# Optimization experiments

Hardware: AMD Instinct MI355X
Metric: run time of the kernel (lower is better)

The kernel has to match this reference:

```python
import jax, jax.numpy as jnp
import numpy as np

N_NODES = 50000
N_EDGES = 800000
IN_DIM = 128
HIDDEN = 64
HEADS = 4
EPS = 1e-5
NEG_SLOPE = 0.2  # PyG GATConv default


def setup_inputs() -> dict:
    key = jax.random.key(0)
    ks = jax.random.split(key, 12)
    s = 0.1
    x = jax.random.normal(ks[0], (N_NODES, IN_DIM), jnp.float32)
    edge_index = jax.random.randint(ks[1], (2, N_EDGES), 0, N_NODES, dtype=jnp.int64)
    return {
        "x": x,
        "edge_index": edge_index,
        # BatchNorm1d(input_dim)
        "gamma1": jnp.ones((IN_DIM,), jnp.float32),
        "beta1": jnp.zeros((IN_DIM,), jnp.float32),
        # GATConv(IN_DIM, HIDDEN, heads=HEADS, concat=True)
        "W1": jax.random.normal(ks[2], (IN_DIM, HEADS * HIDDEN), jnp.float32) * s,
        "att_src1": jax.random.normal(ks[3], (HEADS, HIDDEN), jnp.float32) * s,
        "att_dst1": jax.random.normal(ks[4], (HEADS, HIDDEN), jnp.float32) * s,
        "bias1": jnp.zeros((HEADS * HIDDEN,), jnp.float32),
        # BatchNorm1d(hidden*heads)
        "gamma2": jnp.ones((HEADS * HIDDEN,), jnp.float32),
        "beta2": jnp.zeros((HEADS * HIDDEN,), jnp.float32),
        # GATConv(hidden*heads, HIDDEN, heads=HEADS, concat=False)
        "W2": jax.random.normal(ks[5], (HEADS * HIDDEN, HEADS * HIDDEN), jnp.float32) * s,
        "att_src2": jax.random.normal(ks[6], (HEADS, HIDDEN), jnp.float32) * s,
        "att_dst2": jax.random.normal(ks[7], (HEADS, HIDDEN), jnp.float32) * s,
        "bias2": jnp.zeros((HIDDEN,), jnp.float32),
    }


def batchnorm(x, gamma, beta):
    # training-mode BatchNorm1d: biased variance over the batch dim
    m = x.mean(axis=0)
    v = x.var(axis=0)
    return (x - m) * jax.lax.rsqrt(v + EPS) * gamma + beta


def gat_conv(h, src, dst, W, att_src, att_dst, bias, concat):
    n = h.shape[0]
    hl = (h @ W).reshape(n, HEADS, -1)                 # [N, H, C]
    a_src = (hl * att_src).sum(-1)                     # [N, H]
    a_dst = (hl * att_dst).sum(-1)                     # [N, H]
    e = jax.nn.leaky_relu(a_src[src] + a_dst[dst], NEG_SLOPE)  # [E, H]
    # segment softmax over destination neighborhoods
    e_max = jax.ops.segment_max(e, dst, num_segments=n)
    e = jnp.exp(e - e_max[dst])
    denom = jax.ops.segment_sum(e, dst, num_segments=n)
    alpha = e / denom[dst]                             # [E, H]
    msg = alpha[:, :, None] * hl[src]                  # [E, H, C]
    out = jax.ops.segment_sum(msg, dst, num_segments=n)  # [N, H, C]
    out = out.reshape(n, -1) if concat else out.mean(axis=1)
    return out + bias


def reference(x, edge_index, gamma1, beta1, W1, att_src1, att_dst1, bias1,
              gamma2, beta2, W2, att_src2, att_dst2, bias2):
    n = x.shape[0]
    loop = jnp.arange(n, dtype=edge_index.dtype)
    src = jnp.concatenate([edge_index[0], loop])  # add_self_loops=True
    dst = jnp.concatenate([edge_index[1], loop])
    h = batchnorm(x, gamma1, beta1)
    h = gat_conv(h, src, dst, W1, att_src1, att_dst1, bias1, concat=True)
    h = batchnorm(h, gamma2, beta2)
    h = jax.nn.relu(h)
    h = gat_conv(h, src, dst, W2, att_src2, att_dst2, bias2, concat=False)
    return h
```

## Files before the change

### kernel.cpp

```cpp
#include <hip/hip_runtime.h>

#define N_NODES 50000
#define N_EDGES 800000
#define E_TOT   (N_EDGES + N_NODES)
#define F1      128
#define F2      256
#define EPS     1e-5f
#define SLOPE   0.2f
#define CAP     448
#define SCAN_B  256
#define N_BLKS  ((N_NODES + SCAN_B - 1) / SCAN_B)

typedef __bf16 bf16x8 __attribute__((ext_vector_type(8)));
typedef float  f32x4  __attribute__((ext_vector_type(4)));

__device__ __forceinline__ float bf2f(unsigned short b) {
    return __uint_as_float((unsigned)b << 16);
}

template<int C>
__global__ void bn_stats(const float* __restrict__ X,
                         float* __restrict__ sums, float* __restrict__ sumsq) {
    int t = threadIdx.x;
    float s = 0.f, q = 0.f;
    for (int r = blockIdx.x; r < N_NODES; r += gridDim.x) {
        float v = X[(size_t)r * C + t];
        s += v; q += v * v;
    }
    atomicAdd(&sums[t], s);
    atomicAdd(&sumsq[t], q);
}

__global__ void bn_coef(const float* __restrict__ sums, const float* __restrict__ sumsq,
                        const float* __restrict__ gamma, const float* __restrict__ beta,
                        float* __restrict__ scale, float* __restrict__ shift, int K) {
    int t = blockIdx.x * 64 + threadIdx.x;
    if (t < K) {
        const float invN = 1.f / (float)N_NODES;
        float m  = sums[t] * invN;
        float vv = sumsq[t] * invN - m * m;
        float sc = rsqrtf(vv + EPS) * gamma[t];
        scale[t] = sc;
        shift[t] = fmaf(-m, sc, beta[t]);
    }
}

__global__ void deg_init(int* __restrict__ deg) {
    int i = blockIdx.x * 256 + threadIdx.x;
    if (i < N_NODES) deg[i] = 1;
}
__global__ void deg_count(const int* __restrict__ edst, int* __restrict__ deg) {
    int i = blockIdx.x * 256 + threadIdx.x;
    if (i < N_EDGES) atomicAdd(&deg[edst[i]], 1);
}
__global__ void scan_blocks(const int* __restrict__ deg, int* __restrict__ rowptr,
                            int* __restrict__ bsum) {
    __shared__ int sd[SCAN_B];
    int b = blockIdx.x, t = threadIdx.x;
    int i = b * SCAN_B + t;
    int v = (i < N_NODES) ? deg[i] : 0;
    sd[t] = v;
    __syncthreads();
    for (int off = 1; off < SCAN_B; off <<= 1) {
        int x = (t >= off) ? sd[t - off] : 0;
        __syncthreads();
        sd[t] += x;
        __syncthreads();
    }
    if (i < N_NODES) rowptr[i + 1] = sd[t];
    if (t == SCAN_B - 1) bsum[b] = sd[t];
}
__global__ void scan_totals(int* __restrict__ bsum) {
    __shared__ int sd[SCAN_B];
    int t = threadIdx.x;
    int v = (t < N_BLKS) ? bsum[t] : 0;
    sd[t] = v;
    __syncthreads();
    for (int off = 1; off < SCAN_B; off <<= 1) {
        int x = (t >= off) ? sd[t - off] : 0;
        __syncthreads();
        sd[t] += x;
        __syncthreads();
    }
    if (t < N_BLKS) bsum[t] = sd[t] - v;
}
__global__ void scan_apply(const int* __restrict__ deg, const int* __restrict__ bsum,
                           int* __restrict__ rowptr, int* __restrict__ cursor) {
    int i = blockIdx.x * SCAN_B + threadIdx.x;
    if (i < N_NODES) {
        int r = rowptr[i + 1] + bsum[blockIdx.x];
        rowptr[i + 1] = r;
        cursor[i] = r - deg[i];
        if (i == 0) rowptr[0] = 0;
    }
}
__global__ void fill_csr(const int* __restrict__ esrc, const int* __restrict__ edst,
                         int* __restrict__ cursor, int* __restrict__ col) {
    int i = blockIdx.x * 256 + threadIdx.x;
    if (i < N_EDGES) {
        int p = atomicAdd(&cursor[edst[i]], 1);
        col[p] = esrc[i];
    } else if (i < E_TOT) {
        int n = i - N_EDGES;
        int p = atomicAdd(&cursor[n], 1);
        col[p] = n;
    }
}

template<int K>
__global__ void prep_w(const float* __restrict__ W, __bf16* __restrict__ Wf) {
    int tid = blockIdx.x * 256 + threadIdx.x;
    if (tid >= (K / 32) * 16 * 64) return;
    int lane = tid & 63;
    int nt = (tid >> 6) & 15;
    int ks = tid >> 10;
    int q = lane >> 4, c = lane & 15;
#pragma unroll
    for (int j = 0; j < 8; j++)
        Wf[(size_t)tid * 8 + j] = (__bf16)W[(size_t)(ks * 32 + q * 8 + j) * F2 + nt * 16 + c];
}

template<int K, bool RELU>
__global__ __launch_bounds__(256)
void gemm_mfma(const float* __restrict__ X,
               const float* __restrict__ scale, const float* __restrict__ shift,
               const __bf16* __restrict__ Wf, __bf16* __restrict__ hlb) {
    int t = threadIdx.x;
    int wave = t >> 6, lane = t & 63;
    int q = lane >> 4, c = lane & 15;
    int mrow = (blockIdx.x * 4 + wave) * 32;
    int row0 = mrow + c, row1 = mrow + 16 + c;
    int r0 = row0 < N_NODES ? row0 : N_NODES - 1;
    int r1 = row1 < N_NODES ? row1 : N_NODES - 1;

    f32x4 acc[2][16];
#pragma unroll
    for (int m = 0; m < 2; m++)
#pragma unroll
        for (int nt = 0; nt < 16; nt++) acc[m][nt] = (f32x4){0.f, 0.f, 0.f, 0.f};

    for (int ks = 0; ks < K / 32; ks++) {
        int kb = ks * 32 + q * 8;
        float4 sc0 = *(const float4*)(scale + kb);
        float4 sc1 = *(const float4*)(scale + kb + 4);
        float4 sf0 = *(const float4*)(shift + kb);
        float4 sf1 = *(const float4*)(shift + kb + 4);
        bf16x8 afr[2];
#pragma unroll
        for (int m = 0; m < 2; m++) {
            const float* xp = X + (size_t)(m ? r1 : r0) * K + kb;
            float4 x0 = *(const float4*)xp;
            float4 x1 = *(const float4*)(xp + 4);
            float y0 = fmaf(x0.x, sc0.x, sf0.x);
            float y1 = fmaf(x0.y, sc0.y, sf0.y);
            float y2 = fmaf(x0.z, sc0.z, sf0.z);
            float y3 = fmaf(x0.w, sc0.w, sf0.w);
            float y4 = fmaf(x1.x, sc1.x, sf1.x);
            float y5 = fmaf(x1.y, sc1.y, sf1.y);
            float y6 = fmaf(x1.z, sc1.z, sf1.z);
            float y7 = fmaf(x1.w, sc1.w, sf1.w);
            if (RELU) {
                y0 = fmaxf(y0, 0.f); y1 = fmaxf(y1, 0.f);
                y2 = fmaxf(y2, 0.f); y3 = fmaxf(y3, 0.f);
                y4 = fmaxf(y4, 0.f); y5 = fmaxf(y5, 0.f);
                y6 = fmaxf(y6, 0.f); y7 = fmaxf(y7, 0.f);
            }
            bf16x8 a;
            a[0] = (__bf16)y0; a[1] = (__bf16)y1; a[2] = (__bf16)y2; a[3] = (__bf16)y3;
            a[4] = (__bf16)y4; a[5] = (__bf16)y5; a[6] = (__bf16)y6; a[7] = (__bf16)y7;
            afr[m] = a;
        }
#pragma unroll
        for (int nt = 0; nt < 16; nt++) {
            bf16x8 b = *(const bf16x8*)(Wf + ((size_t)(ks * 16 + nt) * 64 + lane) * 8);
            acc[0][nt] = __builtin_amdgcn_mfma_f32_16x16x32_bf16(afr[0], b, acc[0][nt], 0, 0, 0);
            acc[1][nt] = __builtin_amdgcn_mfma_f32_16x16x32_bf16(afr[1], b, acc[1][nt], 0, 0, 0);
        }
    }
#pragma unroll
    for (int m = 0; m < 2; m++) {
        int rowb = mrow + m * 16 + q * 4;
#pragma unroll
        for (int r = 0; r < 4; r++) {
            int row = rowb + r;
            if (row < N_NODES) {
#pragma unroll
                for (int nt = 0; nt < 16; nt++)
                    hlb[(size_t)row * F2 + nt * 16 + c] = (__bf16)acc[m][nt][r];
            }
        }
    }
}

__global__ __launch_bounds__(256)
void att_dots(const __bf16* __restrict__ hlb,
              const float* __restrict__ att_s, const float* __restrict__ att_d,
              float* __restrict__ a_src, float* __restrict__ a_dst) {
    int t = threadIdx.x;
    int wave = t >> 6, lane = t & 63;
    int n = blockIdx.x * 4 + wave;
    ushort4 hv = ((const ushort4*)(hlb + (size_t)n * F2))[lane];
    float4 as = ((const float4*)att_s)[lane];
    float4 ad = ((const float4*)att_d)[lane];
    float v0 = bf2f(hv.x), v1 = bf2f(hv.y), v2 = bf2f(hv.z), v3 = bf2f(hv.w);
    float vs = v0 * as.x + v1 * as.y + v2 * as.z + v3 * as.w;
    float vd = v0 * ad.x + v1 * ad.y + v2 * ad.z + v3 * ad.w;
#pragma unroll
    for (int off = 1; off < 16; off <<= 1) { vs += __shfl_xor(vs, off); vd += __shfl_xor(vd, off); }
    if ((lane & 15) == 0) {
        int h = lane >> 4;
        a_src[n * 4 + h] = vs;
        a_dst[n * 4 + h] = vd;
    }
}

template<bool MEAN>
__global__ __launch_bounds__(128)
void node_aggr(const int* __restrict__ rowptr, const int* __restrict__ col,
               const float* __restrict__ a_src, const float* __restrict__ a_dst,
               const ushort2* __restrict__ hlb, const float* __restrict__ bias,
               float* __restrict__ out) {
    int n = blockIdx.x, t = threadIdx.x;
    int start = rowptr[n];
    int deg = rowptr[n + 1] - start;
    __shared__ float se[CAP * 4];
    __shared__ int   scol[CAP];
    __shared__ float wred[8];
    __shared__ float sdenom[4];
    int h4 = t & 3;
    float adn = a_dst[n * 4 + h4];
    float local = 0.f;
    bool fits = (deg <= CAP);
    if (fits) {
        for (int i = t; i < deg; i += 128) scol[i] = col[start + i];
        __syncthreads();
        for (int p = t; p < deg * 4; p += 128) {
            int i = p >> 2;
            float v = a_src[scol[i] * 4 + h4] + adn;
            v = v > 0.f ? v : SLOPE * v;
            float e = __expf(v);
            se[p] = e;
            local += e;
        }
    } else {
        for (int p = t; p < deg * 4; p += 128) {
            float v = a_src[col[start + (p >> 2)] * 4 + h4] + adn;
            v = v > 0.f ? v : SLOPE * v;
            local += __expf(v);
        }
    }
#pragma unroll
    for (int off = 4; off < 64; off <<= 1) local += __shfl_xor(local, off);
    if ((t & 63) < 4) wred[(t >> 6) * 4 + h4] = local;
    __syncthreads();
    if (t < 4) sdenom[t] = wred[t] + wred[t + 4];
    __syncthreads();

    int h = t >> 5;
    float rden = 1.f / sdenom[h];
    float acc0 = 0.f, acc1 = 0.f;
    if (fits) {
#pragma unroll 4
        for (int i = 0; i < deg; i++) {
            float alpha = se[i * 4 + h] * rden;
            ushort2 hv = hlb[(size_t)scol[i] * (F2 / 2) + t];
            acc0 = fmaf(alpha, bf2f(hv.x), acc0);
            acc1 = fmaf(alpha, bf2f(hv.y), acc1);
        }
    } else {
        float adh = a_dst[n * 4 + h];
        for (int i = 0; i < deg; i++) {
            int s = col[start + i];
            float v = a_src[s * 4 + h] + adh;
            v = v > 0.f ? v : SLOPE * v;
            float alpha = __expf(v) * rden;
            ushort2 hv = hlb[(size_t)s * (F2 / 2) + t];
            acc0 = fmaf(alpha, bf2f(hv.x), acc0);
            acc1 = fmaf(alpha, bf2f(hv.y), acc1);
        }
    }
    if (MEAN) {
        __shared__ float sred[256];
        sred[2 * t] = acc0; sred[2 * t + 1] = acc1;
        __syncthreads();
        if (t < 64)
            out[(size_t)n * 64 + t] =
                0.25f * (sred[t] + sred[t + 64] + sred[t + 128] + sred[t + 192]) + bias[t];
    } else {
        float2 o; o.x = acc0; o.y = acc1;
        ((float2*)out)[(size_t)n * (F2 / 2) + t] = o;
    }
}

extern "C" void kernel_launch(void* const* d_in, const int* in_sizes, int n_in,
                              void* d_out, int out_size, void* d_ws, size_t ws_size,
                              hipStream_t stream) {
    const float* x        = (const float*)d_in[0];
    const int*   edge     = (const int*)  d_in[1];
    const float* gamma1   = (const float*)d_in[2];
    const float* beta1    = (const float*)d_in[3];
    const float* W1       = (const float*)d_in[4];
    const float* att_src1 = (const float*)d_in[5];
    const float* att_dst1 = (const float*)d_in[6];
    const float* gamma2   = (const float*)d_in[8];
    const float* beta2    = (const float*)d_in[9];
    const float* W2       = (const float*)d_in[10];
    const float* att_src2 = (const float*)d_in[11];
    const float* att_dst2 = (const float*)d_in[12];
    const float* bias2    = (const float*)d_in[13];
    float* out = (float*)d_out;

    const int* esrc = edge;
    const int* edst = edge + N_EDGES;

    float* wsf = (float*)d_ws;
    size_t o = 0;
    __bf16* hlb = (__bf16*)(wsf + o); o += (size_t)N_NODES * F2 / 2;
    float* acc1   = wsf + o; o += (size_t)N_NODES * F2;
    __bf16* Wf1 = (__bf16*)(wsf + o); o += (size_t)F1 * F2 / 2;
    __bf16* Wf2 = (__bf16*)(wsf + o); o += (size_t)F2 * F2 / 2;
    float* a_src1 = wsf + o; o += N_NODES * 4;
    float* a_dst1 = wsf + o; o += N_NODES * 4;
    float* a_src2 = wsf + o; o += N_NODES * 4;
    float* a_dst2 = wsf + o; o += N_NODES * 4;
    float* scale1 = wsf + o; o += F1;
    float* shift1 = wsf + o; o += F1;
    float* scale2 = wsf + o; o += F2;
    float* shift2 = wsf + o; o += F2;
    size_t zstart = o;
    float* sums1  = wsf + o; o += F1;
    float* sumsq1 = wsf + o; o += F1;
    float* sums2  = wsf + o; o += F2;
    float* sumsq2 = wsf + o; o += F2;
    size_t zbytes = (o - zstart) * sizeof(float);
    int* deg    = (int*)(wsf + o); o += N_NODES;
    int* rowptr = (int*)(wsf + o); o += N_NODES + 1;
    int* cursor = (int*)(wsf + o); o += N_NODES;
    int* bsum   = (int*)(wsf + o); o += SCAN_B;
    int* col    = (int*)(wsf + o); o += E_TOT;

    hipMemsetAsync(wsf + zstart, 0, zbytes, stream);

    deg_init   <<<(N_NODES + 255) / 256, 256, 0, stream>>>(deg);
    deg_count  <<<(N_EDGES + 255) / 256, 256, 0, stream>>>(edst, deg);
    scan_blocks<<<N_BLKS, SCAN_B, 0, stream>>>(deg, rowptr, bsum);
    scan_totals<<<1, SCAN_B, 0, stream>>>(bsum);
    scan_apply <<<N_BLKS, SCAN_B, 0, stream>>>(deg, bsum, rowptr, cursor);
    fill_csr   <<<(E_TOT + 255) / 256, 256, 0, stream>>>(esrc, edst, cursor, col);

    prep_w<F1><<<(F1 / 32) * 16 * 64 / 256, 256, 0, stream>>>(W1, Wf1);
    prep_w<F2><<<(F2 / 32) * 16 * 64 / 256, 256, 0, stream>>>(W2, Wf2);

    const int gemm_grid = (N_NODES + 127) / 128;

    bn_stats<F1><<<512, F1, 0, stream>>>(x, sums1, sumsq1);
    bn_coef<<<(F1 + 63) / 64, 64, 0, stream>>>(sums1, sumsq1, gamma1, beta1, scale1, shift1, F1);
    gemm_mfma<F1, false><<<gemm_grid, 256, 0, stream>>>(x, scale1, shift1, Wf1, hlb);
    att_dots<<<N_NODES / 4, 256, 0, stream>>>(hlb, att_src1, att_dst1, a_src1, a_dst1);
    node_aggr<false><<<N_NODES, 128, 0, stream>>>(rowptr, col, a_src1, a_dst1,
                                                  (const ushort2*)hlb, nullptr, acc1);

    bn_stats<F2><<<512, F2, 0, stream>>>(acc1, sums2, sumsq2);
    bn_coef<<<(F2 + 63) / 64, 64, 0, stream>>>(sums2, sumsq2, gamma2, beta2, scale2, shift2, F2);
    gemm_mfma<F2, true><<<gemm_grid, 256, 0, stream>>>(acc1, scale2, shift2, Wf2, hlb);
    att_dots<<<N_NODES / 4, 256, 0, stream>>>(hlb, att_src2, att_dst2, a_src2, a_dst2);
    node_aggr<true><<<N_NODES, 128, 0, stream>>>(rowptr, col, a_src2, a_dst2,
                                                 (const ushort2*)hlb, bias2, out);
}
```

Before: 499.9 us.

## Split GAT aggregation into denominator pass and column-group edge aggregation

Replaces the per-node fused softmax-and-aggregate kernel with a wave-per-node denominator kernel and an aggregation kernel where each block handles 4 nodes for one 32-column group. Attention logits are recomputed per column group instead of being cached in shared memory. This removes the large shared-memory buffers and block-level syncs to raise occupancy and parallelism. In exchange it adds redundant exp/gather work, narrower 2-byte gathers, and an extra combine kernel for the mean head reduction.

```diff
diff --git a/kernel.cpp b/kernel.cpp
--- a/kernel.cpp
+++ b/kernel.cpp
@@ -7,7 +7,6 @@
 #define F2      256
 #define EPS     1e-5f
 #define SLOPE   0.2f
-#define CAP     448
 #define SCAN_B  256
 #define N_BLKS  ((N_NODES + SCAN_B - 1) / SCAN_B)
 
@@ -214,82 +213,77 @@
     }
 }
 
-template<bool MEAN>
-__global__ __launch_bounds__(128)
-void node_aggr(const int* __restrict__ rowptr, const int* __restrict__ col,
-               const float* __restrict__ a_src, const float* __restrict__ a_dst,
-               const ushort2* __restrict__ hlb, const float* __restrict__ bias,
-               float* __restrict__ out) {
-    int n = blockIdx.x, t = threadIdx.x;
+__global__ __launch_bounds__(256)
+void node_denom(const int* __restrict__ rowptr, const int* __restrict__ col,
+                const float* __restrict__ a_src, const float* __restrict__ a_dst,
+                float* __restrict__ rden) {
+    int t = threadIdx.x;
+    int wave = t >> 6, lane = t & 63;
+    int n = blockIdx.x * 4 + wave;
     int start = rowptr[n];
     int deg = rowptr[n + 1] - start;
-    __shared__ float se[CAP * 4];
-    __shared__ int   scol[CAP];
-    __shared__ float wred[8];
-    __shared__ float sdenom[4];
-    int h4 = t & 3;
-    float adn = a_dst[n * 4 + h4];
-    float local = 0.f;
-    bool fits = (deg <= CAP);
-    if (fits) {
-        for (int i = t; i < deg; i += 128) scol[i] = col[start + i];
-        __syncthreads();
-        for (int p = t; p < deg * 4; p += 128) {
-            int i = p >> 2;
-            float v = a_src[scol[i] * 4 + h4] + adn;
-            v = v > 0.f ? v : SLOPE * v;
-            float e = __expf(v);
-            se[p] = e;
-            local += e;
-        }
-    } else {
-        for (int p = t; p < deg * 4; p += 128) {
-            float v = a_src[col[start + (p >> 2)] * 4 + h4] + adn;
-            v = v > 0.f ? v : SLOPE * v;
-            local += __expf(v);
-        }
-    }
-#pragma unroll
-    for (int off = 4; off < 64; off <<= 1) local += __shfl_xor(local, off);
-    if ((t & 63) < 4) wred[(t >> 6) * 4 + h4] = local;
-    __syncthreads();
-    if (t < 4) sdenom[t] = wred[t] + wred[t + 4];
-    __syncthreads();
-
-    int h = t >> 5;
-    float rden = 1.f / sdenom[h];
-    float acc0 = 0.f, acc1 = 0.f;
-    if (fits) {
-#pragma unroll 4
-        for (int i = 0; i < deg; i++) {
-            float alpha = se[i * 4 + h] * rden;
-            ushort2 hv = hlb[(size_t)scol[i] * (F2 / 2) + t];
-            acc0 = fmaf(alpha, bf2f(hv.x), acc0);
-            acc1 = fmaf(alpha, bf2f(hv.y), acc1);
-        }
-    } else {
-        float adh = a_dst[n * 4 + h];
-        for (int i = 0; i < deg; i++) {
-            int s = col[start + i];
-            float v = a_src[s * 4 + h] + adh;
-            v = v > 0.f ? v : SLOPE * v;
-            float alpha = __expf(v) * rden;
-            ushort2 hv = hlb[(size_t)s * (F2 / 2) + t];
-            acc0 = fmaf(alpha, bf2f(hv.x), acc0);
-            acc1 = fmaf(alpha, bf2f(hv.y), acc1);
-        }
-    }
-    if (MEAN) {
-        __shared__ float sred[256];
-        sred[2 * t] = acc0; sred[2 * t + 1] = acc1;
-        __syncthreads();
-        if (t < 64)
-            out[(size_t)n * 64 + t] =
-                0.25f * (sred[t] + sred[t + 64] + sred[t + 128] + sred[t + 192]) + bias[t];
-    } else {
-        float2 o; o.x = acc0; o.y = acc1;
-        ((float2*)out)[(size_t)n * (F2 / 2) + t] = o;
-    }
+    int h = lane & 3;
+    float ad = a_dst[n * 4 + h];
+    float s = 0.f;
+    for (int p = lane; p < deg * 4; p += 64) {
+        int sn = col[start + (p >> 2)];
+        float v = a_src[sn * 4 + h] + ad;
+        v = v > 0.f ? v : SLOPE * v;
+        s += __expf(v);
+    }
+#pragma unroll
+    for (int off = 4; off < 64; off <<= 1) s += __shfl_xor(s, off);
+    if (lane < 4) rden[n * 4 + lane] = 1.f / s;
+}
+
+__global__ __launch_bounds__(256)
+void aggr_split(const int* __restrict__ rowptr, const int* __restrict__ col,
+                const float* __restrict__ a_src, const float* __restrict__ a_dst,
+                const float* __restrict__ rden, const __bf16* __restrict__ hlb,
+                float* __restrict__ outp) {
+    int g = blockIdx.x & 7;
+    int t = threadIdx.x;
+    int wave = t >> 6, lane = t & 63;
+    int n = (blockIdx.x >> 3) * 4 + wave;
+    int sub = lane >> 5, cc = lane & 31;
+    int h = g >> 1;
+    int start = __builtin_nontemporal_load(rowptr + n);
+    int deg   = __builtin_nontemporal_load(rowptr + n + 1) - start;
+    float ad = __builtin_nontemporal_load(a_dst + n * 4 + h);
+    float rd = __builtin_nontemporal_load(rden  + n * 4 + h);
+    const unsigned short* hp = (const unsigned short*)hlb + g * 32 + cc;
+
+    float acc = 0.f;
+    int i = sub;
+    for (; i + 2 < deg; i += 4) {
+        int s0 = __builtin_nontemporal_load(col + start + i);
+        int s1 = __builtin_nontemporal_load(col + start + i + 2);
+        float v0 = a_src[s0 * 4 + h] + ad;
+        float v1 = a_src[s1 * 4 + h] + ad;
+        float f0 = bf2f(hp[(size_t)s0 * F2]);
+        float f1 = bf2f(hp[(size_t)s1 * F2]);
+        v0 = v0 > 0.f ? v0 : SLOPE * v0;
+        v1 = v1 > 0.f ? v1 : SLOPE * v1;
+        acc = fmaf(__expf(v0) * rd, f0, acc);
+        acc = fmaf(__expf(v1) * rd, f1, acc);
+    }
+    for (; i < deg; i += 2) {
+        int s0 = __builtin_nontemporal_load(col + start + i);
+        float v0 = a_src[s0 * 4 + h] + ad;
+        float f0 = bf2f(hp[(size_t)s0 * F2]);
+        v0 = v0 > 0.f ? v0 : SLOPE * v0;
+        acc = fmaf(__expf(v0) * rd, f0, acc);
+    }
+    acc += __shfl_xor(acc, 32);
+    if (sub == 0) outp[(size_t)n * F2 + g * 32 + cc] = acc;
+}
+
+__global__ void combine_mean(const float* __restrict__ p, const float* __restrict__ bias,
+                             float* __restrict__ out) {
+    int i = blockIdx.x * 256 + threadIdx.x;
+    int n = i >> 6, c = i & 63;
+    out[i] = 0.25f * (p[(size_t)n * F2 + c] + p[(size_t)n * F2 + 64 + c] +
+                      p[(size_t)n * F2 + 128 + c] + p[(size_t)n * F2 + 192 + c]) + bias[c];
 }
 
 extern "C" void kernel_launch(void* const* d_in, const int* in_sizes, int n_in,
@@ -323,6 +317,7 @@
     float* a_dst1 = wsf + o; o += N_NODES * 4;
     float* a_src2 = wsf + o; o += N_NODES * 4;
     float* a_dst2 = wsf + o; o += N_NODES * 4;
+    float* rden   = wsf + o; o += N_NODES * 4;
     float* scale1 = wsf + o; o += F1;
     float* shift1 = wsf + o; o += F1;
     float* scale2 = wsf + o; o += F2;
@@ -352,18 +347,20 @@
     prep_w<F2><<<(F2 / 32) * 16 * 64 / 256, 256, 0, stream>>>(W2, Wf2);
 
     const int gemm_grid = (N_NODES + 127) / 128;
+    const int aggr_grid = (N_NODES / 4) * 8;
 
     bn_stats<F1><<<512, F1, 0, stream>>>(x, sums1, sumsq1);
     bn_coef<<<(F1 + 63) / 64, 64, 0, stream>>>(sums1, sumsq1, gamma1, beta1, scale1, shift1, F1);
     gemm_mfma<F1, false><<<gemm_grid, 256, 0, stream>>>(x, scale1, shift1, Wf1, hlb);
     att_dots<<<N_NODES / 4, 256, 0, stream>>>(hlb, att_src1, att_dst1, a_src1, a_dst1);
-    node_aggr<false><<<N_NODES, 128, 0, stream>>>(rowptr, col, a_src1, a_dst1,
-                                                  (const ushort2*)hlb, nullptr, acc1);
+    node_denom<<<N_NODES / 4, 256, 0, stream>>>(rowptr, col, a_src1, a_dst1, rden);
+    aggr_split<<<aggr_grid, 256, 0, stream>>>(rowptr, col, a_src1, a_dst1, rden, hlb, acc1);
 
     bn_stats<F2><<<512, F2, 0, stream>>>(acc1, sums2, sumsq2);
     bn_coef<<<(F2 + 63) / 64, 64, 0, stream>>>(sums2, sumsq2, gamma2, beta2, scale2, shift2, F2);
     gemm_mfma<F2, true><<<gemm_grid, 256, 0, stream>>>(acc1, scale2, shift2, Wf2, hlb);
     att_dots<<<N_NODES / 4, 256, 0, stream>>>(hlb, att_src2, att_dst2, a_src2, a_dst2);
-    node_aggr<true><<<N_NODES, 128, 0, stream>>>(rowptr, col, a_src2, a_dst2,
-                                                 (const ushort2*)hlb, bias2, out);
-}
+    node_denom<<<N_NODES / 4, 256, 0, stream>>>(rowptr, col, a_src2, a_dst2, rden);
+    aggr_split<<<aggr_grid, 256, 0, stream>>>(rowptr, col, a_src2, a_dst2, rden, hlb, acc1);
+    combine_mean<<<N_NODES * 64 / 256, 256, 0, stream>>>(acc1, bias2, out);
+}
```

Result: slower. 1.002 ms (+100.5%).
